# Kernel tuning notes

Measured on AMD Instinct MI355X. Metric: run time of the kernel, lower is better.

The kernel has to match this reference:

```python
import jax, jax.numpy as jnp
import numpy as np

B, S, D, H = 2, 2048, 1024, 16
DH = D // H  # 64

def setup_inputs() -> dict:
    key = jax.random.key(0)
    ks = jax.random.split(key, 12)
    s = 1.0 / np.sqrt(D)
    return {
        "hidden_states": jax.random.normal(ks[0], (B, S, D), jnp.float32),
        "Wq": jax.random.normal(ks[1], (D, D), jnp.float32) * s,
        "bq": jnp.zeros((D,), jnp.float32),
        "Wk": jax.random.normal(ks[2], (D, D), jnp.float32) * s,
        "bk": jnp.zeros((D,), jnp.float32),
        "Wv": jax.random.normal(ks[3], (D, D), jnp.float32) * s,
        "bv": jnp.zeros((D,), jnp.float32),
        "Wo": jax.random.normal(ks[4], (D, D), jnp.float32) * s,
        "bo": jnp.zeros((D,), jnp.float32),
        "gating_factor": jnp.array([0.5], jnp.float32),
        "gating_bias": jax.random.normal(ks[5], (1,), jnp.float32),
    }

def reference(hidden_states, Wq, bq, Wk, bk, Wv, bv, Wo, bo, gating_factor, gating_bias):
    # projections -> [B, S, H, DH]
    q = (hidden_states @ Wq + bq).reshape(B, S, H, DH)
    k = (hidden_states @ Wk + bk).reshape(B, S, H, DH)
    v = (hidden_states @ Wv + bv).reshape(B, S, H, DH)
    # scaled dot-product scores [B, H, S, S]
    scores = jnp.einsum('bqhd,bkhd->bhqk', q, k) / np.sqrt(DH).astype(np.float32)
    probs = jax.nn.softmax(scores, axis=-1)
    # per-(batch, query) gating scalar, broadcast over heads and keys
    gating = jax.nn.sigmoid(gating_factor[0] * hidden_states.mean(axis=-1) + gating_bias[0])  # [B, S]
    probs = probs * gating[:, None, :, None]
    # weighted value sum -> [B, S, D]
    ctx = jnp.einsum('bhqk,bkhd->bqhd', probs, v).reshape(B, S, D)
    return ctx @ Wo + bo
```

## Files before the change

kernel.cpp:

```cpp
#include <hip/hip_runtime.h>
#include <math.h>

#define NB 2
#define NS 2048
#define ND 1024
#define NH 16
#define NDH 64
#define NROWS (NB * NS)

typedef __attribute__((ext_vector_type(8))) short bf16x8;
typedef __attribute__((ext_vector_type(4))) float f32x4;
typedef unsigned short u16;
typedef unsigned int u32;

#define KSCALE 0.18033688011112042f

__device__ __forceinline__ u16 f2bf(float f) {
    u32 u = __float_as_uint(f);
    u += 0x7FFF + ((u >> 16) & 1);
    return (u16)(u >> 16);
}

__device__ __forceinline__ u32 pack_bf2(float lo, float hi) {
    return __builtin_amdgcn_perm(__float_as_uint(hi), __float_as_uint(lo), 0x07060302u);
}

__device__ __forceinline__ void async16(const void* g, const u16* l) {
    __builtin_amdgcn_global_load_lds((const __attribute__((address_space(1))) u32*)g,
                                     (__attribute__((address_space(3))) u32*)l,
                                     16, 0, 0);
}

__global__ __launch_bounds__(256) void gate_kernel(const float* __restrict__ hs,
                                                   const float* __restrict__ gf,
                                                   const float* __restrict__ gb,
                                                   float* __restrict__ gate) {
    const int row = blockIdx.x;
    const int t = threadIdx.x;
    float4 v4 = ((const float4*)(hs + (size_t)row * ND))[t];
    float s = v4.x + v4.y + v4.z + v4.w;
    #pragma unroll
    for (int off = 32; off > 0; off >>= 1) s += __shfl_down(s, off);
    __shared__ float red[4];
    if ((t & 63) == 0) red[t >> 6] = s;
    __syncthreads();
    if (t == 0) {
        float tot = red[0] + red[1] + red[2] + red[3];
        float x = gf[0] * (tot * (1.0f / ND)) + gb[0];
        gate[row] = 1.0f / (1.0f + expf(-x));
    }
}

__global__ __launch_bounds__(256) void hsconv(const float* __restrict__ hs,
                                              u16* __restrict__ hb) {
    size_t base = ((size_t)blockIdx.x * 256 + threadIdx.x) * 8;
    float4 a = *(const float4*)&hs[base];
    float4 b = *(const float4*)&hs[base + 4];
    u16 o[8] = {f2bf(a.x), f2bf(a.y), f2bf(a.z), f2bf(a.w),
                f2bf(b.x), f2bf(b.y), f2bf(b.z), f2bf(b.w)};
    *(uint4*)&hb[base] = *(const uint4*)o;
}

__global__ __launch_bounds__(256) void wtrans(const float* __restrict__ Wq,
                                              const float* __restrict__ Wk,
                                              const float* __restrict__ Wv,
                                              const float* __restrict__ Wo,
                                              u16* __restrict__ out) {
    __shared__ __align__(16) u16 T[64 * 88];
    const int wsel = blockIdx.y;
    const float* W = (wsel == 0) ? Wq : (wsel == 1) ? Wk : (wsel == 2) ? Wv : Wo;
    u16* Wt = out + (size_t)wsel * ND * ND;
    const int tile = blockIdx.x;
    const int k0 = (tile >> 4) * 64, n0 = (tile & 15) * 64;
    const int t = threadIdx.x;
    #pragma unroll
    for (int i = 0; i < 4; ++i) {
        int idx = i * 256 + t;
        int r = idx >> 4, c4 = idx & 15;
        float4 v = *(const float4*)&W[(size_t)(k0 + r) * ND + n0 + c4 * 4];
        T[(c4 * 4 + 0) * 88 + r] = f2bf(v.x);
        T[(c4 * 4 + 1) * 88 + r] = f2bf(v.y);
        T[(c4 * 4 + 2) * 88 + r] = f2bf(v.z);
        T[(c4 * 4 + 3) * 88 + r] = f2bf(v.w);
    }
    __syncthreads();
    #pragma unroll
    for (int i = 0; i < 2; ++i) {
        int slot = i * 256 + t;
        int n = slot >> 3, ch = slot & 7;
        uint4 u = *(const uint4*)&T[n * 88 + ch * 8];
        *(uint4*)&Wt[(size_t)(n0 + n) * ND + k0 + ch * 8] = u;
    }
}

template <int QKV>
__global__ __launch_bounds__(256) void gemm_mfma(
        const u16* __restrict__ A,
        const u16* __restrict__ W0, const u16* __restrict__ W1, const u16* __restrict__ W2,
        const float* __restrict__ b0, const float* __restrict__ b1, const float* __restrict__ b2,
        void* __restrict__ o0, void* __restrict__ o1, void* __restrict__ o2) {
    __shared__ __align__(16) u16 lds[8192];
    const int t = threadIdx.x;
    const int lane = t & 63, wid = t >> 6;
    const int ln = lane & 15, quad = lane >> 4;
    const int wm = wid >> 1, wn = wid & 1;
    const int n0 = blockIdx.x * 128;
    const int m0 = blockIdx.y * 128;
    const int z = QKV ? blockIdx.z : 0;
    const u16* Wt = (z == 0) ? W0 : (z == 1) ? W1 : W2;
    const float* bias = (z == 0) ? b0 : (z == 1) ? b1 : b2;

    f32x4 acc[4][4] = {};
    const int sel = quad ^ ((ln >> 1) & 3);

    for (int k0 = 0; k0 < ND; k0 += 32) {
        #pragma unroll
        for (int i = 0; i < 2; ++i) {
            int slot = i * 256 + t;
            int r = slot >> 2, cp = slot & 3;
            int c = cp ^ ((r >> 1) & 3);
            async16(A + (size_t)(m0 + r) * ND + k0 + c * 8, &lds[slot * 8]);
            async16(Wt + (size_t)(n0 + r) * ND + k0 + c * 8, &lds[4096 + slot * 8]);
        }
        __syncthreads();

        bf16x8 aF[4], bF[4];
        #pragma unroll
        for (int mt = 0; mt < 4; ++mt)
            aF[mt] = *(const bf16x8*)&lds[(wm * 64 + mt * 16 + ln) * 32 + sel * 8];
        #pragma unroll
        for (int nt = 0; nt < 4; ++nt)
            bF[nt] = *(const bf16x8*)&lds[4096 + (wn * 64 + nt * 16 + ln) * 32 + sel * 8];
        #pragma unroll
        for (int mt = 0; mt < 4; ++mt)
            #pragma unroll
            for (int nt = 0; nt < 4; ++nt)
                acc[mt][nt] = __builtin_amdgcn_mfma_f32_16x16x32_bf16(aF[mt], bF[nt], acc[mt][nt], 0, 0, 0);
        __syncthreads();
    }

    float bv[4];
    #pragma unroll
    for (int nt = 0; nt < 4; ++nt) bv[nt] = bias[n0 + wn * 64 + nt * 16 + ln];
    const float osc = (QKV == 1 && z == 0) ? KSCALE : 1.0f;

    if (QKV == 0) {
        float* out = (float*)o0;
        #pragma unroll
        for (int mt = 0; mt < 4; ++mt)
            #pragma unroll
            for (int nt = 0; nt < 4; ++nt)
                #pragma unroll
                for (int r = 0; r < 4; ++r)
                    out[(size_t)(m0 + wm * 64 + mt * 16 + quad * 4 + r) * ND +
                        n0 + wn * 64 + nt * 16 + ln] = acc[mt][nt][r] + bv[nt];
    } else if (z <= 1) {
        u16* out = (u16*)(z == 0 ? o0 : o1);
        #pragma unroll
        for (int mt = 0; mt < 4; ++mt)
            #pragma unroll
            for (int nt = 0; nt < 4; ++nt)
                #pragma unroll
                for (int r = 0; r < 4; ++r)
                    out[(size_t)(m0 + wm * 64 + mt * 16 + quad * 4 + r) * ND +
                        n0 + wn * 64 + nt * 16 + ln] = f2bf((acc[mt][nt][r] + bv[nt]) * osc);
    } else {
        u16* vt = (u16*)o2;
        #pragma unroll
        for (int mt = 0; mt < 4; ++mt)
            #pragma unroll
            for (int nt = 0; nt < 4; ++nt) {
                int gcol = n0 + wn * 64 + nt * 16 + ln;
                int head = gcol >> 6, dh = gcol & 63;
                #pragma unroll
                for (int r = 0; r < 4; ++r) {
                    int grow = m0 + wm * 64 + mt * 16 + quad * 4 + r;
                    int bb = grow >> 11, s = grow & (NS - 1);
                    vt[((size_t)(bb * NH + head) * NDH + dh) * NS + s] =
                        f2bf(acc[mt][nt][r] + bv[nt]);
                }
            }
    }
}

__global__ __launch_bounds__(256) void attn_mfma(const u16* __restrict__ Q,
                                                 const u16* __restrict__ K,
                                                 const u16* __restrict__ Vt,
                                                 const float* __restrict__ gate,
                                                 u16* __restrict__ ctx) {
    __shared__ __align__(16) u16 Ks[64 * 64];
    __shared__ __align__(16) u16 Vs[64 * 64];
    __shared__ __align__(16) u16 Ps[4][32 * 72];

    const int t = threadIdx.x;
    const int wid = t >> 6;
    const int lane = t & 63;
    const int ln = lane & 15;
    const int quad = lane >> 4;
    const int sw = ln & 7;

    const int q0 = blockIdx.x * 128;
    const int h  = blockIdx.y;
    const int b  = blockIdx.z;
    const size_t rowbase = (size_t)b * NS;

    bf16x8 aQ[2][2];
    #pragma unroll
    for (int mt = 0; mt < 2; ++mt) {
        const u16* qrow = Q + (rowbase + q0 + wid * 32 + mt * 16 + ln) * ND + h * NDH;
        aQ[mt][0] = *(const bf16x8*)(qrow + quad * 8);
        aQ[mt][1] = *(const bf16x8*)(qrow + quad * 8 + 32);
    }

    const short one = 0x3F80;
    const bf16x8 vOnes = {one, one, one, one, one, one, one, one};

    f32x4 acc[2][5] = {};

    const int sr = t >> 3;
    const int scp = t & 7;
    const u16* kbase = K + rowbase * ND + h * NDH;
    const u16* vbase = Vt + (size_t)(b * NH + h) * NDH * NS;

    for (int k0 = 0; k0 < NS; k0 += 64) {
        #pragma unroll
        for (int i = 0; i < 2; ++i) {
            int slot = i * 256 + t;
            int r = sr + i * 32;
            int c = scp ^ (r & 7);
            async16(kbase + (size_t)(k0 + r) * ND + c * 8, &Ks[slot * 8]);
            async16(vbase + (size_t)r * NS + k0 + c * 8, &Vs[slot * 8]);
        }
        __syncthreads();

        bf16x8 kF[4][2];
        #pragma unroll
        for (int g = 0; g < 4; ++g) {
            kF[g][0] = *(const bf16x8*)&Ks[(16 * g + ln) * 64 + ((quad + 0) ^ sw) * 8];
            kF[g][1] = *(const bf16x8*)&Ks[(16 * g + ln) * 64 + ((quad + 4) ^ sw) * 8];
        }

        u16* pw = Ps[wid];
        #pragma unroll
        for (int mt = 0; mt < 2; ++mt) {
            f32x4 cS[4];
            #pragma unroll
            for (int g = 0; g < 4; ++g) {
                f32x4 z = {0.f, 0.f, 0.f, 0.f};
                z = __builtin_amdgcn_mfma_f32_16x16x32_bf16(kF[g][0], aQ[mt][0], z, 0, 0, 0);
                cS[g] = __builtin_amdgcn_mfma_f32_16x16x32_bf16(kF[g][1], aQ[mt][1], z, 0, 0, 0);
            }
            #pragma unroll
            for (int g = 0; g < 4; ++g) {
                float p0 = exp2f(cS[g][0]), p1 = exp2f(cS[g][1]);
                float p2 = exp2f(cS[g][2]), p3 = exp2f(cS[g][3]);
                uint2 pk;
                pk.x = pack_bf2(p0, p1);
                pk.y = pack_bf2(p2, p3);
                *(uint2*)&pw[(mt * 16 + ln) * 72 + g * 16 + quad * 4] = pk;
            }
        }

        __asm__ volatile("s_waitcnt lgkmcnt(0)" ::: "memory");

        bf16x8 vF[4][2];
        #pragma unroll
        for (int g = 0; g < 4; ++g) {
            vF[g][0] = *(const bf16x8*)&Vs[(16 * g + ln) * 64 + ((quad + 0) ^ sw) * 8];
            vF[g][1] = *(const bf16x8*)&Vs[(16 * g + ln) * 64 + ((quad + 4) ^ sw) * 8];
        }
        #pragma unroll
        for (int mt = 0; mt < 2; ++mt) {
            #pragma unroll
            for (int hf = 0; hf < 2; ++hf) {
                bf16x8 aP = *(const bf16x8*)&pw[(mt * 16 + ln) * 72 + quad * 8 + 32 * hf];
                #pragma unroll
                for (int g = 0; g < 4; ++g)
                    acc[mt][g] = __builtin_amdgcn_mfma_f32_16x16x32_bf16(aP, vF[g][hf], acc[mt][g], 0, 0, 0);
                acc[mt][4] = __builtin_amdgcn_mfma_f32_16x16x32_bf16(aP, vOnes, acc[mt][4], 0, 0, 0);
            }
        }
        __syncthreads();
    }

    #pragma unroll
    for (int mt = 0; mt < 2; ++mt)
        #pragma unroll
        for (int r = 0; r < 4; ++r) {
            int row = q0 + wid * 32 + mt * 16 + quad * 4 + r;
            float g = gate[rowbase + row];
            float sc = g / acc[mt][4][r];
            u16* orow = ctx + (rowbase + row) * ND + h * NDH;
            #pragma unroll
            for (int gg = 0; gg < 4; ++gg)
                orow[16 * gg + ln] = f2bf(acc[mt][gg][r] * sc);
        }
}

extern "C" void kernel_launch(void* const* d_in, const int* in_sizes, int n_in,
                              void* d_out, int out_size, void* d_ws, size_t ws_size,
                              hipStream_t stream) {
    (void)in_sizes; (void)n_in; (void)out_size; (void)ws_size;
    const float* hs = (const float*)d_in[0];
    const float* Wq = (const float*)d_in[1];
    const float* bq = (const float*)d_in[2];
    const float* Wk = (const float*)d_in[3];
    const float* bk = (const float*)d_in[4];
    const float* Wv = (const float*)d_in[5];
    const float* bv = (const float*)d_in[6];
    const float* Wo = (const float*)d_in[7];
    const float* bo = (const float*)d_in[8];
    const float* gf = (const float*)d_in[9];
    const float* gb = (const float*)d_in[10];
    float* out = (float*)d_out;

    char* ws = (char*)d_ws;
    const size_t M1 = 1u << 20;
    u16*   hsb  = (u16*)(ws);
    u16*   wt   = (u16*)(ws + 8 * M1);
    u16*   q    = (u16*)(ws + 16 * M1);
    u16*   k    = (u16*)(ws + 24 * M1);
    u16*   vt   = (u16*)(ws + 32 * M1);
    u16*   ctxb = (u16*)(ws + 40 * M1);
    float* gate = (float*)(ws + 48 * M1);

    u16* wqt = wt;
    u16* wkt = wt + (size_t)ND * ND;
    u16* wvt = wt + 2 * (size_t)ND * ND;
    u16* wot = wt + 3 * (size_t)ND * ND;

    dim3 blk(256);
    gate_kernel<<<dim3(NROWS), blk, 0, stream>>>(hs, gf, gb, gate);
    hsconv<<<dim3(2048), blk, 0, stream>>>(hs, hsb);
    wtrans<<<dim3(256, 4), blk, 0, stream>>>(Wq, Wk, Wv, Wo, wt);

    gemm_mfma<1><<<dim3(ND / 128, NROWS / 128, 3), blk, 0, stream>>>(
        hsb, wqt, wkt, wvt, bq, bk, bv, q, k, vt);

    attn_mfma<<<dim3(NS / 128, NH, NB), blk, 0, stream>>>(q, k, vt, gate, ctxb);

    gemm_mfma<0><<<dim3(ND / 128, NROWS / 128, 1), blk, 0, stream>>>(
        ctxb, wot, nullptr, nullptr, bo, nullptr, nullptr, out, nullptr, nullptr);
}
```

Before: 242.4 us.

## Split attention key range across two wave groups and fuse gate with bf16 conversion

The attention kernel now runs 512 threads per block. Two groups of four waves each process half of the key sequence with separate K/V shared buffers, and their partial numerators and denominators are combined through shared memory at the end. The change doubles in-flight waves per query tile to raise latency hiding, at the cost of more shared memory and an extra reduction step. The gate computation is also fused into the hidden-state bf16 conversion kernel, saving one read of the input and one launch. exp2f is replaced with the hardware exp2 builtin.

Result: faster. 210.0 us (-13.4%).

```diff
diff --git a/kernel.cpp b/kernel.cpp
--- a/kernel.cpp
+++ b/kernel.cpp
@@ -25,40 +25,39 @@
     return __builtin_amdgcn_perm(__float_as_uint(hi), __float_as_uint(lo), 0x07060302u);
 }
 
+__device__ __forceinline__ float fast_exp2(float x) {
+    return __builtin_amdgcn_exp2f(x);
+}
+
 __device__ __forceinline__ void async16(const void* g, const u16* l) {
     __builtin_amdgcn_global_load_lds((const __attribute__((address_space(1))) u32*)g,
                                      (__attribute__((address_space(3))) u32*)l,
                                      16, 0, 0);
 }
 
-__global__ __launch_bounds__(256) void gate_kernel(const float* __restrict__ hs,
-                                                   const float* __restrict__ gf,
-                                                   const float* __restrict__ gb,
-                                                   float* __restrict__ gate) {
+__global__ __launch_bounds__(128) void gatehs(const float* __restrict__ hs,
+                                              const float* __restrict__ gf,
+                                              const float* __restrict__ gb,
+                                              u16* __restrict__ hb,
+                                              float* __restrict__ gate) {
     const int row = blockIdx.x;
     const int t = threadIdx.x;
-    float4 v4 = ((const float4*)(hs + (size_t)row * ND))[t];
-    float s = v4.x + v4.y + v4.z + v4.w;
-    #pragma unroll
-    for (int off = 32; off > 0; off >>= 1) s += __shfl_down(s, off);
-    __shared__ float red[4];
-    if ((t & 63) == 0) red[t >> 6] = s;
-    __syncthreads();
-    if (t == 0) {
-        float tot = red[0] + red[1] + red[2] + red[3];
-        float x = gf[0] * (tot * (1.0f / ND)) + gb[0];
-        gate[row] = 1.0f / (1.0f + expf(-x));
-    }
-}
-
-__global__ __launch_bounds__(256) void hsconv(const float* __restrict__ hs,
-                                              u16* __restrict__ hb) {
-    size_t base = ((size_t)blockIdx.x * 256 + threadIdx.x) * 8;
+    size_t base = (size_t)row * ND + t * 8;
     float4 a = *(const float4*)&hs[base];
     float4 b = *(const float4*)&hs[base + 4];
     u16 o[8] = {f2bf(a.x), f2bf(a.y), f2bf(a.z), f2bf(a.w),
                 f2bf(b.x), f2bf(b.y), f2bf(b.z), f2bf(b.w)};
     *(uint4*)&hb[base] = *(const uint4*)o;
+    float s = a.x + a.y + a.z + a.w + b.x + b.y + b.z + b.w;
+    #pragma unroll
+    for (int off = 32; off > 0; off >>= 1) s += __shfl_down(s, off);
+    __shared__ float red[2];
+    if ((t & 63) == 0) red[t >> 6] = s;
+    __syncthreads();
+    if (t == 0) {
+        float x = gf[0] * ((red[0] + red[1]) * (1.0f / ND)) + gb[0];
+        gate[row] = 1.0f / (1.0f + expf(-x));
+    }
 }
 
 __global__ __launch_bounds__(256) void wtrans(const float* __restrict__ Wq,
@@ -183,20 +182,21 @@
     }
 }
 
-__global__ __launch_bounds__(256) void attn_mfma(const u16* __restrict__ Q,
+__global__ __launch_bounds__(512) void attn_mfma(const u16* __restrict__ Q,
                                                  const u16* __restrict__ K,
                                                  const u16* __restrict__ Vt,
                                                  const float* __restrict__ gate,
                                                  u16* __restrict__ ctx) {
-    __shared__ __align__(16) u16 Ks[64 * 64];
-    __shared__ __align__(16) u16 Vs[64 * 64];
-    __shared__ __align__(16) u16 Ps[4][32 * 72];
+    __shared__ __align__(16) u16 kv[4][4096];
+    __shared__ __align__(16) u16 ps[8][2304];
 
     const int t = threadIdx.x;
     const int wid = t >> 6;
     const int lane = t & 63;
     const int ln = lane & 15;
     const int quad = lane >> 4;
+    const int kh = wid >> 2;
+    const int wq = wid & 3;
     const int sw = ln & 7;
 
     const int q0 = blockIdx.x * 128;
@@ -207,7 +207,7 @@
     bf16x8 aQ[2][2];
     #pragma unroll
     for (int mt = 0; mt < 2; ++mt) {
-        const u16* qrow = Q + (rowbase + q0 + wid * 32 + mt * 16 + ln) * ND + h * NDH;
+        const u16* qrow = Q + (rowbase + q0 + wq * 32 + mt * 16 + ln) * ND + h * NDH;
         aQ[mt][0] = *(const bf16x8*)(qrow + quad * 8);
         aQ[mt][1] = *(const bf16x8*)(qrow + quad * 8 + 32);
     }
@@ -217,15 +217,20 @@
 
     f32x4 acc[2][5] = {};
 
-    const int sr = t >> 3;
-    const int scp = t & 7;
+    const int tl = t & 255;
+    const int sr = tl >> 3;
+    const int scp = tl & 7;
     const u16* kbase = K + rowbase * ND + h * NDH;
     const u16* vbase = Vt + (size_t)(b * NH + h) * NDH * NS;
-
-    for (int k0 = 0; k0 < NS; k0 += 64) {
+    u16* Ks = kv[kh];
+    u16* Vs = kv[2 + kh];
+    u16* pw = ps[wid];
+
+    for (int kt = 0; kt < 16; ++kt) {
+        const int k0 = kh * 1024 + kt * 64;
         #pragma unroll
         for (int i = 0; i < 2; ++i) {
-            int slot = i * 256 + t;
+            int slot = i * 256 + tl;
             int r = sr + i * 32;
             int c = scp ^ (r & 7);
             async16(kbase + (size_t)(k0 + r) * ND + c * 8, &Ks[slot * 8]);
@@ -240,7 +245,6 @@
             kF[g][1] = *(const bf16x8*)&Ks[(16 * g + ln) * 64 + ((quad + 4) ^ sw) * 8];
         }
 
-        u16* pw = Ps[wid];
         #pragma unroll
         for (int mt = 0; mt < 2; ++mt) {
             f32x4 cS[4];
@@ -252,8 +256,8 @@
             }
             #pragma unroll
             for (int g = 0; g < 4; ++g) {
-                float p0 = exp2f(cS[g][0]), p1 = exp2f(cS[g][1]);
-                float p2 = exp2f(cS[g][2]), p3 = exp2f(cS[g][3]);
+                float p0 = fast_exp2(cS[g][0]), p1 = fast_exp2(cS[g][1]);
+                float p2 = fast_exp2(cS[g][2]), p3 = fast_exp2(cS[g][3]);
                 uint2 pk;
                 pk.x = pack_bf2(p0, p1);
                 pk.y = pack_bf2(p2, p3);
@@ -283,18 +287,40 @@
         __syncthreads();
     }
 
-    #pragma unroll
-    for (int mt = 0; mt < 2; ++mt)
-        #pragma unroll
-        for (int r = 0; r < 4; ++r) {
-            int row = q0 + wid * 32 + mt * 16 + quad * 4 + r;
-            float g = gate[rowbase + row];
-            float sc = g / acc[mt][4][r];
-            u16* orow = ctx + (rowbase + row) * ND + h * NDH;
-            #pragma unroll
-            for (int gg = 0; gg < 4; ++gg)
-                orow[16 * gg + ln] = f2bf(acc[mt][gg][r] * sc);
-        }
+    float* Obuf = (float*)kv;
+    float* Lbuf = (float*)ps;
+
+    if (kh == 1) {
+        #pragma unroll
+        for (int mt = 0; mt < 2; ++mt) {
+            #pragma unroll
+            for (int r = 0; r < 4; ++r) {
+                int lrow = wq * 32 + mt * 16 + quad * 4 + r;
+                #pragma unroll
+                for (int gg = 0; gg < 4; ++gg)
+                    Obuf[lrow * 64 + 16 * gg + ln] = acc[mt][gg][r];
+                if (ln == 0) Lbuf[lrow] = acc[mt][4][r];
+            }
+        }
+    }
+    __syncthreads();
+    if (kh == 0) {
+        #pragma unroll
+        for (int mt = 0; mt < 2; ++mt)
+            #pragma unroll
+            for (int r = 0; r < 4; ++r) {
+                int lrow = wq * 32 + mt * 16 + quad * 4 + r;
+                int row = q0 + lrow;
+                float l = acc[mt][4][r] + Lbuf[lrow];
+                float g = gate[rowbase + row];
+                float sc = g / l;
+                u16* orow = ctx + (rowbase + row) * ND + h * NDH;
+                #pragma unroll
+                for (int gg = 0; gg < 4; ++gg)
+                    orow[16 * gg + ln] =
+                        f2bf((acc[mt][gg][r] + Obuf[lrow * 64 + 16 * gg + ln]) * sc);
+            }
+    }
 }
 
 extern "C" void kernel_launch(void* const* d_in, const int* in_sizes, int n_in,
@@ -329,16 +355,14 @@
     u16* wvt = wt + 2 * (size_t)ND * ND;
     u16* wot = wt + 3 * (size_t)ND * ND;
 
-    dim3 blk(256);
-    gate_kernel<<<dim3(NROWS), blk, 0, stream>>>(hs, gf, gb, gate);
-    hsconv<<<dim3(2048), blk, 0, stream>>>(hs, hsb);
-    wtrans<<<dim3(256, 4), blk, 0, stream>>>(Wq, Wk, Wv, Wo, wt);
-
-    gemm_mfma<1><<<dim3(ND / 128, NROWS / 128, 3), blk, 0, stream>>>(
+    gatehs<<<dim3(NROWS), dim3(128), 0, stream>>>(hs, gf, gb, hsb, gate);
+    wtrans<<<dim3(256, 4), dim3(256), 0, stream>>>(Wq, Wk, Wv, Wo, wt);
+
+    gemm_mfma<1><<<dim3(ND / 128, NROWS / 128, 3), dim3(256), 0, stream>>>(
         hsb, wqt, wkt, wvt, bq, bk, bv, q, k, vt);
 
-    attn_mfma<<<dim3(NS / 128, NH, NB), blk, 0, stream>>>(q, k, vt, gate, ctxb);
-
-    gemm_mfma<0><<<dim3(ND / 128, NROWS / 128, 1), blk, 0, stream>>>(
+    attn_mfma<<<dim3(NS / 128, NH, NB), dim3(512), 0, stream>>>(q, k, vt, gate, ctxb);
+
+    gemm_mfma<0><<<dim3(ND / 128, NROWS / 128, 1), dim3(256), 0, stream>>>(
         ctxb, wot, nullptr, nullptr, bo, nullptr, nullptr, out, nullptr, nullptr);
 }
```
